# Optimization experiments

Measured on AMD Instinct MI355X. Metric: run time of the kernel, lower is better.

The kernel has to match this reference:

```python
import jax, jax.numpy as jnp
import numpy as np

R, NU, NM, E = 5, 100000, 100000, 1000000
IN, MSG, OUT, BAS = 64, 80, 64, 4
MPR = MSG // R  # per-rating message units (stack agg)


def setup_inputs() -> dict:
    key = jax.random.key(0)
    ks = jax.random.split(key, 12)
    return {
        "ufeat": jax.random.normal(ks[0], (NU, IN), jnp.float32),
        "ifeat": jax.random.normal(ks[1], (NM, IN), jnp.float32),
        "cj_user": jax.random.uniform(ks[2], (NU, 1), jnp.float32) + 0.1,
        "ci_user": jax.random.uniform(ks[3], (NU, 1), jnp.float32) + 0.1,
        "cj_movie": jax.random.uniform(ks[4], (NM, 1), jnp.float32) + 0.1,
        "ci_movie": jax.random.uniform(ks[5], (NM, 1), jnp.float32) + 0.1,
        "edge_user": jax.random.randint(ks[6], (R, E), 0, NU, jnp.int32),
        "edge_movie": jax.random.randint(ks[7], (R, E), 0, NM, jnp.int32),
        "att": jax.random.normal(ks[8], (R, BAS), jnp.float32),
        "basis": jax.random.normal(ks[9], (BAS, IN, MPR), jnp.float32),
        "fc_w": jax.random.normal(ks[10], (OUT, MSG), jnp.float32) / np.sqrt(MSG),
        "fc_b": jnp.zeros((OUT,), jnp.float32),
    }


def _agg(feat, src, dst, cj, ci, n_dst):
    # gather src features scaled by cj, scatter-sum to dst, scale by ci
    m = feat[src] * cj[src]                                 # [E, MPR]
    out = jax.ops.segment_sum(m, dst, num_segments=n_dst)   # [n_dst, MPR]
    return out * ci


def reference(ufeat, ifeat, cj_user, ci_user, cj_movie, ci_movie,
              edge_user, edge_movie, att, basis, fc_w, fc_b):
    # per-rating weights from basis decomposition
    W = jnp.einsum('rb,bio->rio', att, basis)       # [R, IN, MPR]
    fu = jnp.einsum('ni,rio->rno', ufeat, W)        # [R, NU, MPR]
    fi = jnp.einsum('ni,rio->rno', ifeat, W)        # [R, NM, MPR]
    agg = jax.vmap(_agg, in_axes=(0, 0, 0, None, None, None))
    # forward edges: user -> movie; reverse edges: movie -> user
    m_out = agg(fu, edge_user, edge_movie, cj_user, ci_movie, NM)  # [R, NM, MPR]
    u_out = agg(fi, edge_movie, edge_user, cj_movie, ci_user, NU)  # [R, NU, MPR]
    # 'stack' cross-type aggregation, flattened over ratings
    u = jnp.transpose(u_out, (1, 0, 2)).reshape(NU, MSG)
    m = jnp.transpose(m_out, (1, 0, 2)).reshape(NM, MSG)
    u = jax.nn.relu(u) @ fc_w.T + fc_b   # shared ufc == ifc
    m = jax.nn.relu(m) @ fc_w.T + fc_b
    return u, m
```

## Files before the change

kernel.cpp:

```cpp
#include <hip/hip_runtime.h>
#include <cstdint>
#include <cstddef>

constexpr int kR   = 5;
constexpr int kNU  = 100000;
constexpr int kNM  = 100000;
constexpr int kE   = 1000000;
constexpr int kIN  = 64;
constexpr int kMSG = 80;
constexpr int kOUT = 64;
constexpr int kBAS = 4;
constexpr int kMPR = 16;

constexpr int kN        = 100000;
constexpr unsigned kEdges   = (unsigned)kR * (unsigned)kE;

constexpr int kBD        = 50;
constexpr int kNB        = kN / kBD;

constexpr int kNC        = 2;
constexpr unsigned kPlanesPerChunk = 250000;
constexpr int kBinsPerDir = kNB * kNC;
constexpr unsigned kCap2 = 1536;
constexpr int kChunkE    = 16384;
constexpr int kDirBlocks = (int)((kEdges + kChunkE - 1) / kChunkE);
constexpr int kMsgBlocks = (kN + 255) / 256;

constexpr float kScale    = 64.0f;
constexpr float kInvScale = 1.0f / 64.0f;

constexpr int kStride = 17;
constexpr int kAccWords = kBD * kR * kStride;

__global__ __launch_bounds__(256) void gcmc_init(
    uint32_t* __restrict__ cursor, const float* __restrict__ fc_w,
    float* __restrict__ Wq)
{
    const int t = blockIdx.x * 256 + threadIdx.x;
    if (t < 2 * kBinsPerDir) cursor[t] = (uint32_t)t * kCap2;
    if (t < 20 * kOUT * 4) {
        const int q  = t & 3;
        const int o  = (t >> 2) & 63;
        const int j4 = t >> 8;
        Wq[t] = fc_w[o * kMSG + j4 * 4 + q];
    }
}

__device__ __forceinline__ uint32_t pack2i16(float x, float y) {
    const int ix = (int)rintf(fminf(fmaxf(x, -32760.f), 32760.f));
    const int iy = (int)rintf(fminf(fmaxf(y, -32760.f), 32760.f));
    return (uint32_t)(ix & 0xFFFF) | ((uint32_t)(iy & 0xFFFF) << 16);
}

__global__ __launch_bounds__(256) void gcmc_msg(
    const float* __restrict__ ufeat, const float* __restrict__ ifeat,
    const float* __restrict__ cj_user, const float* __restrict__ cj_movie,
    const float* __restrict__ att,  const float* __restrict__ basis,
    short* __restrict__ ms)
{
    __shared__ float Wl[kR * kIN * kMPR];
    const int tid  = threadIdx.x;
    const int side = blockIdx.x >= kMsgBlocks;
    const int blk  = blockIdx.x - side * kMsgBlocks;
    const float* feat = side ? ifeat : ufeat;
    const float* cj   = side ? cj_movie : cj_user;
    uint2* mout = reinterpret_cast<uint2*>(ms + (side ? (size_t)kR * kN * kMPR : 0));

    for (int idx = tid; idx < kR * kIN * kMPR; idx += 256) {
        const int r   = idx >> 10;
        const int rem = idx & 1023;
        const int i   = rem >> 4;
        const int k   = rem & 15;
        float s = 0.f;
#pragma unroll
        for (int b = 0; b < kBAS; ++b)
            s += att[r * kBAS + b] * basis[(b * kIN + i) * kMPR + k];
        Wl[idx] = s;
    }
    __syncthreads();

    const int node = blk * 256 + tid;
    if (node >= kN) return;

    float f[kIN];
    const float4* fp = reinterpret_cast<const float4*>(feat + (size_t)node * kIN);
#pragma unroll
    for (int i = 0; i < kIN / 4; ++i) {
        float4 v = fp[i];
        f[4 * i + 0] = v.x; f[4 * i + 1] = v.y;
        f[4 * i + 2] = v.z; f[4 * i + 3] = v.w;
    }
    const float c = cj[node] * kScale;
    const float4* W4 = reinterpret_cast<const float4*>(Wl);

    for (int r = 0; r < kR; ++r) {
#pragma unroll
        for (int kg = 0; kg < kMPR / 4; ++kg) {
            float4 a = make_float4(0.f, 0.f, 0.f, 0.f);
#pragma unroll
            for (int i = 0; i < kIN; ++i) {
                float4 w = W4[(r * kIN + i) * (kMPR / 4) + kg];
                a.x += f[i] * w.x; a.y += f[i] * w.y;
                a.z += f[i] * w.z; a.w += f[i] * w.w;
            }
            const uint32_t plane = (uint32_t)(r * kN + node);
            mout[plane * 4u + kg] =
                make_uint2(pack2i16(a.x * c, a.y * c), pack2i16(a.z * c, a.w * c));
        }
    }
}

__global__ __launch_bounds__(1024) void gcmc_partition(
    const int* __restrict__ dst0, const int* __restrict__ src0,
    const int* __restrict__ dst1, const int* __restrict__ src1,
    uint32_t* __restrict__ cursor, uint32_t* __restrict__ bucket_recs)
{
    __shared__ uint32_t hist[kBinsPerDir];
    __shared__ uint32_t excl[kBinsPerDir];
    __shared__ uint32_t scanT[1024];
    __shared__ uint32_t stage[kChunkE];
    __shared__ uint16_t sbkt[kChunkE];
    const int tid = threadIdx.x;
    const int dir = blockIdx.x >= kDirBlocks;
    const int blk = blockIdx.x - dir * kDirBlocks;
    const int* dsts = dir ? dst1 : dst0;
    const int* srcs = dir ? src1 : src0;

    for (int i = tid; i < kBinsPerDir; i += 1024) hist[i] = 0;
    __syncthreads();

    const unsigned base = (unsigned)blk * kChunkE;
    uint32_t rec[16], bk[16], rk[16];
#pragma unroll
    for (int j = 0; j < 16; ++j) {
        const unsigned idx = base + j * 1024u + tid;
        if (idx < kEdges) {
            const unsigned d = (unsigned)dsts[idx];
            const unsigned s = (unsigned)srcs[idx];
            const unsigned r = idx / (unsigned)kE;
            const unsigned b = d / (unsigned)kBD;
            const unsigned dl = d - b * (unsigned)kBD;
            const unsigned plane = r * (unsigned)kN + s;
            const unsigned ch = plane / kPlanesPerChunk;
            const unsigned binl = b * (unsigned)kNC + ch;
            rec[j] = plane | (((dl * (unsigned)kR + r) * 17u) << 19);
            bk[j]  = binl;
            rk[j]  = atomicAdd(&hist[binl], 1u);
        } else bk[j] = 0xFFFFFFFFu;
    }
    __syncthreads();

    uint32_t loc[4]; uint32_t s2 = 0;
#pragma unroll
    for (int q = 0; q < 4; ++q) {
        const int b = tid * 4 + q;
        loc[q] = (b < kBinsPerDir) ? hist[b] : 0u;
        s2 += loc[q];
    }
    scanT[tid] = s2; __syncthreads();
    for (int off = 1; off < 1024; off <<= 1) {
        const uint32_t v = (tid >= off) ? scanT[tid - off] : 0u;
        __syncthreads();
        scanT[tid] += v;
        __syncthreads();
    }
    const uint32_t total = scanT[1023];
    uint32_t run = scanT[tid] - s2;
#pragma unroll
    for (int q = 0; q < 4; ++q) {
        const int b = tid * 4 + q;
        if (b < kBinsPerDir) {
            excl[b] = run;
            hist[b] = loc[q] ? atomicAdd(&cursor[dir * kBinsPerDir + b], loc[q]) : 0u;
        }
        run += loc[q];
    }
    __syncthreads();

#pragma unroll
    for (int j = 0; j < 16; ++j) {
        if (bk[j] != 0xFFFFFFFFu) {
            const uint32_t p = excl[bk[j]] + rk[j];
            stage[p] = rec[j];
            sbkt[p]  = (uint16_t)bk[j];
        }
    }
    __syncthreads();

    for (unsigned p = tid; p < total; p += 1024) {
        const uint32_t b = sbkt[p];
        bucket_recs[hist[b] + (p - excl[b])] = stage[p];
    }
}

__global__ __launch_bounds__(256, 8) void gcmc_accum_fc(
    const short* __restrict__ ms,
    const uint32_t* __restrict__ bucket_recs,
    const uint32_t* __restrict__ cursor,
    const float* __restrict__ ci_user, const float* __restrict__ ci_movie,
    const float* __restrict__ Wq, const float* __restrict__ fc_b,
    float* __restrict__ out_u, float* __restrict__ out_m)
{
    __shared__ int accI[kAccWords];
    const int tid = threadIdx.x;
    const int db  = blockIdx.x;
    const int dir = db >= kNB;
    const int bl  = db - dir * kNB;

    for (int i = tid; i < kAccWords; i += 256) accI[i] = 0;
    __syncthreads();

    const uint4* pb = reinterpret_cast<const uint4*>(
        ms + (dir ? (size_t)kR * kN * kMPR : 0));

#define RRR(IDX) { const uint32_t rc = rp[(IDX)];                           \
                   const uint4* lp = pb + (size_t)(rc & 0x7FFFFu) * 2u;      \
                   const uint4 va = lp[0];                                   \
                   const uint4 vb = lp[1];                                   \
                   const int w = (int)(rc >> 19);                            \
                   atomicAdd(&accI[w+ 0], (int)(short)va.x);                 \
                   atomicAdd(&accI[w+ 1], ((int)va.x) >> 16);                \
                   atomicAdd(&accI[w+ 2], (int)(short)va.y);                 \
                   atomicAdd(&accI[w+ 3], ((int)va.y) >> 16);                \
                   atomicAdd(&accI[w+ 4], (int)(short)va.z);                 \
                   atomicAdd(&accI[w+ 5], ((int)va.z) >> 16);                \
                   atomicAdd(&accI[w+ 6], (int)(short)va.w);                 \
                   atomicAdd(&accI[w+ 7], ((int)va.w) >> 16);                \
                   atomicAdd(&accI[w+ 8], (int)(short)vb.x);                 \
                   atomicAdd(&accI[w+ 9], ((int)vb.x) >> 16);                \
                   atomicAdd(&accI[w+10], (int)(short)vb.y);                 \
                   atomicAdd(&accI[w+11], ((int)vb.y) >> 16);                \
                   atomicAdd(&accI[w+12], (int)(short)vb.z);                 \
                   atomicAdd(&accI[w+13], ((int)vb.z) >> 16);                \
                   atomicAdd(&accI[w+14], (int)(short)vb.w);                 \
                   atomicAdd(&accI[w+15], ((int)vb.w) >> 16); }

    for (int ch = 0; ch < kNC; ++ch) {
        const int bin = (dir * kBinsPerDir) + bl * kNC + ch;
        const uint32_t b0 = (uint32_t)bin * kCap2;
        const uint32_t n  = cursor[bin] - b0;
        const uint32_t* rp = bucket_recs + b0;
        uint32_t i = (uint32_t)tid;
        for (; i + 768u < n; i += 1024u) { RRR(i) RRR(i + 256u) RRR(i + 512u) RRR(i + 768u) }
        for (; i < n; i += 256u) { RRR(i) }
    }
#undef RRR
    __syncthreads();

    const int o = tid & 63;
    const int w4 = tid >> 6;
    const float* cip = dir ? ci_user : ci_movie;
    float* outp      = dir ? out_u  : out_m;
    const int dstBase = bl * kBD;
    const float bo = fc_b[o];
    const float4* Wq4 = reinterpret_cast<const float4*>(Wq);

    for (int dl = w4; dl < kBD; dl += 4) {
        const float cs = cip[dstBase + dl] * kInvScale;
        float a = bo;
#pragma unroll 4
        for (int j4 = 0; j4 < kMSG / 4; ++j4) {
            const int base2 = (dl * kR + (j4 >> 2)) * kStride + ((j4 & 3) << 2);
            const float x0 = fmaxf((float)accI[base2 + 0] * cs, 0.f);
            const float x1 = fmaxf((float)accI[base2 + 1] * cs, 0.f);
            const float x2 = fmaxf((float)accI[base2 + 2] * cs, 0.f);
            const float x3 = fmaxf((float)accI[base2 + 3] * cs, 0.f);
            const float4 wv = Wq4[j4 * 64 + o];
            a += x0 * wv.x + x1 * wv.y + x2 * wv.z + x3 * wv.w;
        }
        outp[(size_t)(dstBase + dl) * kOUT + o] = a;
    }
}

extern "C" void kernel_launch(void* const* d_in, const int* in_sizes, int n_in,
                              void* d_out, int out_size, void* d_ws, size_t ws_size,
                              hipStream_t stream) {
    const float* ufeat    = (const float*)d_in[0];
    const float* ifeat    = (const float*)d_in[1];
    const float* cj_user  = (const float*)d_in[2];
    const float* ci_user  = (const float*)d_in[3];
    const float* cj_movie = (const float*)d_in[4];
    const float* ci_movie = (const float*)d_in[5];
    const int*   edge_user  = (const int*)d_in[6];
    const int*   edge_movie = (const int*)d_in[7];
    const float* att   = (const float*)d_in[8];
    const float* basis = (const float*)d_in[9];
    const float* fc_w  = (const float*)d_in[10];
    const float* fc_b  = (const float*)d_in[11];

    float* out_u = (float*)d_out;
    float* out_m = out_u + (size_t)kNU * kOUT;

    short* ms = (short*)d_ws;
    uint32_t* bucket_recs = (uint32_t*)(ms + (size_t)2 * kR * kN * kMPR);
    uint32_t* cursorC     = bucket_recs + (size_t)(2 * kBinsPerDir) * kCap2;
    float*    Wq          = (float*)(cursorC + 2 * kBinsPerDir);

    gcmc_init<<<40, 256, 0, stream>>>(cursorC, fc_w, Wq);

    gcmc_msg<<<2 * kMsgBlocks, 256, 0, stream>>>(
        ufeat, ifeat, cj_user, cj_movie, att, basis, ms);

    gcmc_partition<<<2 * kDirBlocks, 1024, 0, stream>>>(
        edge_movie, edge_user, edge_user, edge_movie, cursorC, bucket_recs);

    gcmc_accum_fc<<<2 * kNB, 256, 0, stream>>>(
        ms, bucket_recs, cursorC, ci_user, ci_movie,
        Wq, fc_b, out_u, out_m);
}
```

Measured before the change: 350.3 us.

## Use FP16 MFMA for message projection, wave-shuffle scan, precompute relu-scaled accumulators

```diff
diff --git a/kernel.cpp b/kernel.cpp
--- a/kernel.cpp
+++ b/kernel.cpp
@@ -24,13 +24,19 @@
 constexpr unsigned kCap2 = 1536;
 constexpr int kChunkE    = 16384;
 constexpr int kDirBlocks = (int)((kEdges + kChunkE - 1) / kChunkE);
-constexpr int kMsgBlocks = (kN + 255) / 256;
 
 constexpr float kScale    = 64.0f;
 constexpr float kInvScale = 1.0f / 64.0f;
 
 constexpr int kStride = 17;
 constexpr int kAccWords = kBD * kR * kStride;
+
+constexpr int kMsgTile   = 256;
+constexpr int kMsgBlocks = (kN + kMsgTile - 1) / kMsgTile;
+constexpr int kWallStride = 72;
+
+typedef _Float16 half8  __attribute__((ext_vector_type(8)));
+typedef float    floatx4 __attribute__((ext_vector_type(4)));
 
 __global__ __launch_bounds__(256) void gcmc_init(
     uint32_t* __restrict__ cursor, const float* __restrict__ fc_w,
@@ -46,68 +52,99 @@
     }
 }
 
-__device__ __forceinline__ uint32_t pack2i16(float x, float y) {
-    const int ix = (int)rintf(fminf(fmaxf(x, -32760.f), 32760.f));
-    const int iy = (int)rintf(fminf(fmaxf(y, -32760.f), 32760.f));
-    return (uint32_t)(ix & 0xFFFF) | ((uint32_t)(iy & 0xFFFF) << 16);
-}
-
 __global__ __launch_bounds__(256) void gcmc_msg(
     const float* __restrict__ ufeat, const float* __restrict__ ifeat,
     const float* __restrict__ cj_user, const float* __restrict__ cj_movie,
     const float* __restrict__ att,  const float* __restrict__ basis,
     short* __restrict__ ms)
 {
-    __shared__ float Wl[kR * kIN * kMPR];
+    __shared__ _Float16 WallT[kMSG * kWallStride];
     const int tid  = threadIdx.x;
     const int side = blockIdx.x >= kMsgBlocks;
     const int blk  = blockIdx.x - side * kMsgBlocks;
     const float* feat = side ? ifeat : ufeat;
     const float* cj   = side ? cj_movie : cj_user;
-    uint2* mout = reinterpret_cast<uint2*>(ms + (side ? (size_t)kR * kN * kMPR : 0));
-
-    for (int idx = tid; idx < kR * kIN * kMPR; idx += 256) {
-        const int r   = idx >> 10;
-        const int rem = idx & 1023;
-        const int i   = rem >> 4;
-        const int k   = rem & 15;
+    short* mbase = ms + (side ? (size_t)kR * kN * kMPR : 0);
+
+    for (int e = tid; e < kMSG * kIN; e += 256) {
+        const int c  = e >> 6;
+        const int i  = e & 63;
+        const int r  = c >> 4;
+        const int kk = c & 15;
         float s = 0.f;
 #pragma unroll
         for (int b = 0; b < kBAS; ++b)
-            s += att[r * kBAS + b] * basis[(b * kIN + i) * kMPR + k];
-        Wl[idx] = s;
-    }
-    __syncthreads();
-
-    const int node = blk * 256 + tid;
-    if (node >= kN) return;
-
-    float f[kIN];
-    const float4* fp = reinterpret_cast<const float4*>(feat + (size_t)node * kIN);
-#pragma unroll
-    for (int i = 0; i < kIN / 4; ++i) {
-        float4 v = fp[i];
-        f[4 * i + 0] = v.x; f[4 * i + 1] = v.y;
-        f[4 * i + 2] = v.z; f[4 * i + 3] = v.w;
-    }
-    const float c = cj[node] * kScale;
-    const float4* W4 = reinterpret_cast<const float4*>(Wl);
-
-    for (int r = 0; r < kR; ++r) {
-#pragma unroll
-        for (int kg = 0; kg < kMPR / 4; ++kg) {
-            float4 a = make_float4(0.f, 0.f, 0.f, 0.f);
-#pragma unroll
-            for (int i = 0; i < kIN; ++i) {
-                float4 w = W4[(r * kIN + i) * (kMPR / 4) + kg];
-                a.x += f[i] * w.x; a.y += f[i] * w.y;
-                a.z += f[i] * w.z; a.w += f[i] * w.w;
+            s += att[r * kBAS + b] * basis[(b * kIN + i) * kMPR + kk];
+        WallT[c * kWallStride + i] = (_Float16)s;
+    }
+    __syncthreads();
+
+    const int lane = tid & 63;
+    const int wv   = tid >> 6;
+    const int lr   = lane & 15;
+    const int lg   = lane >> 4;
+    const int node0w = blk * kMsgTile + wv * 64;
+
+    half8 bf[5][2];
+#pragma unroll
+    for (int nt = 0; nt < 5; ++nt)
+#pragma unroll
+        for (int kh = 0; kh < 2; ++kh)
+            bf[nt][kh] = *reinterpret_cast<const half8*>(
+                &WallT[(nt * 16 + lr) * kWallStride + kh * 32 + lg * 8]);
+
+    int   rowA[4]; float cjs[4];
+#pragma unroll
+    for (int m = 0; m < 4; ++m) {
+        const int n = node0w + m * 16 + lr;
+        rowA[m] = n < kN ? n : kN - 1;
+        cjs[m]  = cj[rowA[m]] * kScale;
+    }
+
+    floatx4 acc[4][5];
+#pragma unroll
+    for (int m = 0; m < 4; ++m)
+#pragma unroll
+        for (int nt = 0; nt < 5; ++nt) {
+            acc[m][nt][0] = 0.f; acc[m][nt][1] = 0.f;
+            acc[m][nt][2] = 0.f; acc[m][nt][3] = 0.f;
+        }
+
+#pragma unroll
+    for (int kh = 0; kh < 2; ++kh) {
+#pragma unroll
+        for (int m = 0; m < 4; ++m) {
+            const float4* fp = reinterpret_cast<const float4*>(
+                feat + (size_t)rowA[m] * kIN + kh * 32 + lg * 8);
+            const float4 f0 = fp[0];
+            const float4 f1 = fp[1];
+            const float cs = cjs[m];
+            half8 am;
+            am[0] = (_Float16)(f0.x * cs); am[1] = (_Float16)(f0.y * cs);
+            am[2] = (_Float16)(f0.z * cs); am[3] = (_Float16)(f0.w * cs);
+            am[4] = (_Float16)(f1.x * cs); am[5] = (_Float16)(f1.y * cs);
+            am[6] = (_Float16)(f1.z * cs); am[7] = (_Float16)(f1.w * cs);
+#pragma unroll
+            for (int nt = 0; nt < 5; ++nt)
+                acc[m][nt] = __builtin_amdgcn_mfma_f32_16x16x32_f16(
+                    am, bf[nt][kh], acc[m][nt], 0, 0, 0);
+        }
+    }
+
+#pragma unroll
+    for (int m = 0; m < 4; ++m)
+#pragma unroll
+        for (int reg = 0; reg < 4; ++reg) {
+            const int node = node0w + m * 16 + lg * 4 + reg;
+            if (node < kN) {
+#pragma unroll
+                for (int nt = 0; nt < 5; ++nt) {
+                    float v = acc[m][nt][reg];
+                    v = fminf(fmaxf(v, -32760.f), 32760.f);
+                    mbase[((size_t)nt * kN + node) * kMPR + lr] = (short)rintf(v);
+                }
             }
-            const uint32_t plane = (uint32_t)(r * kN + node);
-            mout[plane * 4u + kg] =
-                make_uint2(pack2i16(a.x * c, a.y * c), pack2i16(a.z * c, a.w * c));
-        }
-    }
+        }
 }
 
 __global__ __launch_bounds__(1024) void gcmc_partition(
@@ -117,7 +154,7 @@
 {
     __shared__ uint32_t hist[kBinsPerDir];
     __shared__ uint32_t excl[kBinsPerDir];
-    __shared__ uint32_t scanT[1024];
+    __shared__ uint32_t wsum[17];
     __shared__ uint32_t stage[kChunkE];
     __shared__ uint16_t sbkt[kChunkE];
     const int tid = threadIdx.x;
@@ -157,15 +194,24 @@
         loc[q] = (b < kBinsPerDir) ? hist[b] : 0u;
         s2 += loc[q];
     }
-    scanT[tid] = s2; __syncthreads();
-    for (int off = 1; off < 1024; off <<= 1) {
-        const uint32_t v = (tid >= off) ? scanT[tid - off] : 0u;
-        __syncthreads();
-        scanT[tid] += v;
-        __syncthreads();
-    }
-    const uint32_t total = scanT[1023];
-    uint32_t run = scanT[tid] - s2;
+    uint32_t inc = s2;
+    const int lane = tid & 63;
+#pragma unroll
+    for (int d = 1; d < 64; d <<= 1) {
+        const uint32_t t = __shfl_up(inc, d);
+        if (lane >= d) inc += t;
+    }
+    if (lane == 63) wsum[tid >> 6] = inc;
+    __syncthreads();
+    if (tid == 0) {
+        uint32_t run0 = 0;
+#pragma unroll
+        for (int w = 0; w < 16; ++w) { const uint32_t c = wsum[w]; wsum[w] = run0; run0 += c; }
+        wsum[16] = run0;
+    }
+    __syncthreads();
+    const uint32_t total = wsum[16];
+    uint32_t run = wsum[tid >> 6] + (inc - s2);
 #pragma unroll
     for (int q = 0; q < 4; ++q) {
         const int b = tid * 4 + q;
@@ -247,24 +293,35 @@
 #undef RRR
     __syncthreads();
 
+    const float* cip = dir ? ci_user : ci_movie;
+    const int dstBase = bl * kBD;
+    float* accF = reinterpret_cast<float*>(accI);
+    for (int e = tid; e < kAccWords; e += 256) {
+        const int q = e / kStride;
+        const int w = e - q * kStride;
+        if (w < 16) {
+            const int dl = q / kR;
+            const float cs = cip[dstBase + dl] * kInvScale;
+            accF[e] = fmaxf((float)accI[e] * cs, 0.f);
+        }
+    }
+    __syncthreads();
+
     const int o = tid & 63;
     const int w4 = tid >> 6;
-    const float* cip = dir ? ci_user : ci_movie;
-    float* outp      = dir ? out_u  : out_m;
-    const int dstBase = bl * kBD;
+    float* outp = dir ? out_u : out_m;
     const float bo = fc_b[o];
     const float4* Wq4 = reinterpret_cast<const float4*>(Wq);
 
     for (int dl = w4; dl < kBD; dl += 4) {
-        const float cs = cip[dstBase + dl] * kInvScale;
         float a = bo;
 #pragma unroll 4
         for (int j4 = 0; j4 < kMSG / 4; ++j4) {
             const int base2 = (dl * kR + (j4 >> 2)) * kStride + ((j4 & 3) << 2);
-            const float x0 = fmaxf((float)accI[base2 + 0] * cs, 0.f);
-            const float x1 = fmaxf((float)accI[base2 + 1] * cs, 0.f);
-            const float x2 = fmaxf((float)accI[base2 + 2] * cs, 0.f);
-            const float x3 = fmaxf((float)accI[base2 + 3] * cs, 0.f);
+            const float x0 = accF[base2 + 0];
+            const float x1 = accF[base2 + 1];
+            const float x2 = accF[base2 + 2];
+            const float x3 = accF[base2 + 3];
             const float4 wv = Wq4[j4 * 64 + o];
             a += x0 * wv.x + x1 * wv.y + x2 * wv.z + x3 * wv.w;
         }
```

After: 343.0 us. -2.1%, faster.
